# Optimization experiments

Measured on AMD Instinct MI355X. Metric: run time of the kernel, lower is better.

## Reference

```python
import jax, jax.numpy as jnp
import numpy as np

N = 10000        # nodes
E = 160000       # edges (before self-loops)
NFEAT = 256
NHID = 128
H = 4            # heads
NCLASS = 40
NLAYERS = 2
DT = 1.0
ALPHA = 1.0
GAMMA = 1.0
NEG_SLOPE = 0.2  # GATConv leaky_relu slope


def setup_inputs() -> dict:
    key = jax.random.key(0)
    ks = jax.random.split(key, 12)

    def glorot(k, shape):
        fan_in, fan_out = shape[-1], shape[0]
        lim = (6.0 / (fan_in + fan_out)) ** 0.5
        return jax.random.uniform(k, shape, jnp.float32, -lim, lim)

    return {
        "x": jax.random.normal(ks[0], (N, NFEAT), jnp.float32),
        "edge_index": jax.random.randint(ks[1], (2, E), 0, N, jnp.int64),
        "enc_w": glorot(ks[2], (NHID, NFEAT)),
        "enc_b": jnp.zeros((NHID,), jnp.float32),
        "res_w": glorot(ks[3], (H * NHID, NHID)),
        "res_b": jnp.zeros((H * NHID,), jnp.float32),
        "gat_w": glorot(ks[4], (H * NHID, NHID)),
        "att_src": glorot(ks[5], (H, NHID)) * 0.1,
        "att_dst": glorot(ks[6], (H, NHID)) * 0.1,
        "gat_b": jnp.zeros((H * NHID,), jnp.float32),
        "dec_w": glorot(ks[7], (NCLASS, NHID)),
        "dec_b": jnp.zeros((NCLASS,), jnp.float32),
    }


def _gat_conv(x, src, dst, gat_w, att_src, att_dst, gat_b):
    # x: [N, NHID] -> per-head features [N, H, C]
    xh = (x @ gat_w.T).reshape(N, H, NHID)
    a_src = jnp.sum(xh * att_src[None], axis=-1)  # [N, H]
    a_dst = jnp.sum(xh * att_dst[None], axis=-1)  # [N, H]
    e = jax.nn.leaky_relu(a_src[src] + a_dst[dst], NEG_SLOPE)  # [E', H]
    # segment softmax over incoming edges of each destination node
    m = jax.ops.segment_max(e, dst, num_segments=N)            # [N, H]
    e = jnp.exp(e - m[dst])
    s = jax.ops.segment_sum(e, dst, num_segments=N)            # [N, H]
    alpha = e / s[dst]                                          # [E', H]
    msg = xh[src] * alpha[:, :, None]                           # [E', H, C]
    out = jax.ops.segment_sum(msg, dst, num_segments=N)         # [N, H, C]
    return out.reshape(N, H * NHID) + gat_b


def reference(x, edge_index, enc_w, enc_b, res_w, res_b, gat_w,
              att_src, att_dst, gat_b, dec_w, dec_b):
    # add self-loops (GATConv default)
    loop = jnp.arange(N, dtype=edge_index.dtype)
    src = jnp.concatenate([edge_index[0], loop])
    dst = jnp.concatenate([edge_index[1], loop])

    Y = jax.nn.relu(x @ enc_w.T + enc_b)  # [N, NHID]
    X = Y
    for _ in range(NLAYERS):
        conv = _gat_conv(X, src, dst, gat_w, att_src, att_dst, gat_b)  # [N, H*NHID]
        res = X @ res_w.T + res_b                                       # [N, H*NHID]
        # faithful to .view(n_nodes, -1, nheads).mean(-1): [N, NHID, H] -> mean over heads axis
        z = jax.nn.elu(conv + res).reshape(N, NHID, H).mean(axis=-1)    # [N, NHID]
        Y = Y + DT * (z - ALPHA * Y - GAMMA * X)
        X = X + DT * Y
    return X @ dec_w.T + dec_b  # [N, NCLASS]
```

## Files before the change

### kernel.cpp

```cpp
#include <hip/hip_runtime.h>
#include <math.h>

#define NN 10000
#define EE 160000
#define EP 170000
#define NFEAT 256
#define NHID 128
#define NH 4
#define HF 512
#define NCLASS 40

typedef __attribute__((ext_vector_type(8))) short bf8;
typedef __attribute__((ext_vector_type(8))) unsigned short u16x8;
typedef __attribute__((ext_vector_type(4))) float f4;

__device__ __forceinline__ float leaky02(float x) { return x >= 0.0f ? x : 0.2f * x; }

__device__ __forceinline__ unsigned short f2bf(float f) {
    unsigned u = __builtin_bit_cast(unsigned, f);
    unsigned r = (u + 0x7FFF + ((u >> 16) & 1)) >> 16;
    return (unsigned short)r;
}
__device__ __forceinline__ float bf2f(unsigned short h) {
    return __builtin_bit_cast(float, (unsigned)h << 16);
}

__device__ __forceinline__ int swz(int row, int c) {
    return ((((c >> 3) ^ (row & 7)) << 3) | (c & 7));
}

__device__ __forceinline__ void gl_lds16(const unsigned short* g, unsigned short* l)
{
    __builtin_amdgcn_global_load_lds(
        (const __attribute__((address_space(1))) unsigned int*)g,
        (__attribute__((address_space(3))) unsigned int*)l, 16, 0, 0);
}

#define CVT_EL 136192
#define CVT_B  67
#define TOT_B  188

__global__ __launch_bounds__(256)
void fused0_k(const float* __restrict__ gat_w, const float* __restrict__ res_w,
              const float* __restrict__ dec_w,
              const float* __restrict__ res_b, const float* __restrict__ gat_b,
              const int* __restrict__ ei,
              unsigned short* __restrict__ fwhi, unsigned short* __restrict__ dwhi,
              float* __restrict__ biasRG, int* __restrict__ cnt)
{
    int bId = blockIdx.x, t = threadIdx.x;
    if (bId < CVT_B) {
        int iu = bId * 256 + t;
        int i = iu * 8;
        if (i >= CVT_EL) return;
        const float* src; unsigned short* ph; int j;
        if (i < 131072) { j = i;          ph = fwhi;
                          src = (j < 65536) ? (gat_w + j) : (res_w + j - 65536); }
        else            { j = i - 131072; ph = dwhi; src = dec_w + j; }
        int row = j >> 7, c = j & 127;
        float4 v0 = *(const float4*)src, v1 = *(const float4*)(src + 4);
        float vv[8] = {v0.x, v0.y, v0.z, v0.w, v1.x, v1.y, v1.z, v1.w};
        unsigned short hs[8];
#pragma unroll
        for (int k = 0; k < 8; ++k) hs[k] = f2bf(vv[k]);
        *(u16x8*)(ph + row * 128 + swz(row, c)) = *(u16x8*)hs;
    } else if (bId == CVT_B) {
        biasRG[t]       = res_b[t]       + gat_b[t];
        biasRG[t + 256] = res_b[t + 256] + gat_b[t + 256];
    } else {
        for (int e = (bId - CVT_B - 1) * 256 + t; e < EP; e += (TOT_B - CVT_B - 1) * 256) {
            int d = (e < EE) ? ei[EE + e] : (e - EE);
            atomicAdd(&cnt[d], 1);
        }
    }
}

template<int MODE, int KTILES, int MERGE, bool F32>
__global__ __launch_bounds__(256)
void gemm3_k(const void* __restrict__ Ap, const void* __restrict__ Bp,
             const float* __restrict__ bias, float* __restrict__ outF,
             unsigned short* __restrict__ outH, unsigned short* __restrict__ outL,
             float* __restrict__ aS, float* __restrict__ aD,
             const float* __restrict__ attS, const float* __restrict__ attD, int M,
             const int* __restrict__ ei, const int* __restrict__ cnt,
             int* __restrict__ row_ptr, int* __restrict__ cursor, int* __restrict__ csr)
{
    constexpr int K = KTILES * 128;
    __shared__ __align__(16) unsigned short smem[2 * 64 * 128];
    const int tid = threadIdx.x;

    if (MERGE && blockIdx.y == gridDim.y - 1) {
        if (MERGE == 1) {
            if (blockIdx.x != 0) return;
            int* smi = (int*)smem;
            int i0 = tid * 40, i1 = min(i0 + 40, NN);
            int part = 0;
            for (int i = i0; i < i1; ++i) part += cnt[i];
            smi[tid] = part;
            __syncthreads();
            for (int off = 1; off < 256; off <<= 1) {
                int v = (tid >= off) ? smi[tid - off] : 0;
                __syncthreads();
                smi[tid] += v;
                __syncthreads();
            }
            int run = smi[tid] - part;
            for (int i = i0; i < i1; ++i) { row_ptr[i] = run; run += cnt[i]; }
            if (tid == 255) row_ptr[NN] = run;
        } else {
            int stride = gridDim.x * 256;
            for (int e = blockIdx.x * 256 + tid; e < EP; e += stride) {
                int s, d;
                if (e < EE) { s = ei[e]; d = ei[EE + e]; } else { s = e - EE; d = s; }
                int pos = row_ptr[d] + atomicAdd(&cursor[d], 1);
                csr[pos] = s;
            }
        }
        return;
    }

    unsigned short* sA = smem;
    unsigned short* sB = smem + 8192;

    const int lane = tid & 63, wv = tid >> 6;
    const int wr = (wv >> 1) * 32, wc = (wv & 1) * 32;
    const int bm = blockIdx.x * 64, bn = blockIdx.y * 64;
    const int r16 = lane & 15, q4 = lane >> 4;

    f4 acc[2][2];
#pragma unroll
    for (int i = 0; i < 2; ++i)
#pragma unroll
        for (int j = 0; j < 2; ++j) acc[i][j] = (f4){0.f, 0.f, 0.f, 0.f};

    const int ra0 = wr + r16;
    const int rb0 = wc + r16;

    for (int kt = 0; kt < KTILES; ++kt) {
        if (kt) __syncthreads();
        if (!F32) {
            const unsigned short* A = (const unsigned short*)Ap;
            const unsigned short* B = (const unsigned short*)Bp;
#pragma unroll
            for (int j = 0; j < 4; ++j) {
                int i = tid + j * 256;
                int row = i >> 4, u = i & 15;
                int arow = min(bm + row, M - 1);
                size_t ga = (size_t)arow * K + kt * 128 + u * 8;
                size_t gb = (size_t)(bn + row) * K + kt * 128 + u * 8;
                int lb = (wv * 64 + j * 256) * 8;
                gl_lds16(A + ga, sA + lb);
                gl_lds16(B + gb, sB + lb);
            }
        } else {
            const float* A = (const float*)Ap;
            const float* B = (const float*)Bp;
#pragma unroll
            for (int j = 0; j < 4; ++j) {
                int i = tid + j * 256;
                int row = i >> 4, u = i & 15;
                int arow = min(bm + row, M - 1);
                const float* pa = A + (size_t)arow * K + kt * 128 + u * 8;
                const float* pb = B + (size_t)(bn + row) * K + kt * 128 + u * 8;
                float4 a0 = *(const float4*)pa, a1 = *(const float4*)(pa + 4);
                float4 b0 = *(const float4*)pb, b1 = *(const float4*)(pb + 4);
                float av[8] = {a0.x, a0.y, a0.z, a0.w, a1.x, a1.y, a1.z, a1.w};
                float bv[8] = {b0.x, b0.y, b0.z, b0.w, b1.x, b1.y, b1.z, b1.w};
                unsigned short ha[8], hb[8];
#pragma unroll
                for (int k = 0; k < 8; ++k) { ha[k] = f2bf(av[k]); hb[k] = f2bf(bv[k]); }
                int off = row * 128 + ((u ^ (row & 7)) * 8);
                *(u16x8*)(sA + off) = *(u16x8*)ha;
                *(u16x8*)(sB + off) = *(u16x8*)hb;
            }
        }
        __syncthreads();

#pragma unroll
        for (int ks = 0; ks < 4; ++ks) {
            int u = ks * 4 + q4;
            int oa0 = ra0 * 128 + ((u ^ (ra0 & 7)) * 8);
            int ob0 = rb0 * 128 + ((u ^ (rb0 & 7)) * 8);
            int oa1 = oa0 + 16 * 128;
            int ob1 = ob0 + 16 * 128;
            bf8 A0 = *(const bf8*)(sA + oa0);
            bf8 A1 = *(const bf8*)(sA + oa1);
            bf8 B0 = *(const bf8*)(sB + ob0);
            bf8 B1 = *(const bf8*)(sB + ob1);

            acc[0][0] = __builtin_amdgcn_mfma_f32_16x16x32_bf16(A0, B0, acc[0][0], 0, 0, 0);
            acc[0][1] = __builtin_amdgcn_mfma_f32_16x16x32_bf16(A0, B1, acc[0][1], 0, 0, 0);
            acc[1][0] = __builtin_amdgcn_mfma_f32_16x16x32_bf16(A1, B0, acc[1][0], 0, 0, 0);
            acc[1][1] = __builtin_amdgcn_mfma_f32_16x16x32_bf16(A1, B1, acc[1][1], 0, 0, 0);
        }
    }

    const int rbase = q4 * 4;

    if (MODE == 0) {
#pragma unroll
        for (int i = 0; i < 2; ++i)
#pragma unroll
            for (int j = 0; j < 2; ++j)
#pragma unroll
                for (int r = 0; r < 4; ++r) {
                    int row = bm + wr + i * 16 + rbase + r;
                    int col = bn + wc + j * 16 + r16;
                    if (row >= M || col >= NCLASS) continue;
                    outF[(size_t)row * NCLASS + col] = acc[i][j][r] + bias[col];
                }
        return;
    }

    __syncthreads();
    float* sC = (float*)smem;
#pragma unroll
    for (int i = 0; i < 2; ++i)
#pragma unroll
        for (int j = 0; j < 2; ++j)
#pragma unroll
            for (int r = 0; r < 4; ++r)
                sC[(wr + i * 16 + rbase + r) * 65 + (wc + j * 16 + r16)] = acc[i][j][r];
    __syncthreads();

    int row = tid >> 2, seg = tid & 3, c0 = seg * 16;
    int grow = bm + row;
    if (grow < M) {
        float v[16];
#pragma unroll
        for (int k = 0; k < 16; ++k) v[k] = sC[row * 65 + c0 + k];

        if (MODE == 1) {
            unsigned short hs[16];
#pragma unroll
            for (int k = 0; k < 16; ++k)
                hs[k] = f2bf(fmaxf(v[k] + bias[bn + c0 + k], 0.0f));
#pragma unroll
            for (int uu = 0; uu < 2; ++uu) {
                int ug = (bn + c0) / 8 + uu;
                int pu = ug ^ (grow & 7);
                *(u16x8*)(outH + (size_t)grow * 128 + pu * 8) = *(u16x8*)(hs + uu * 8);
            }
        } else {
            if (bn < 512) {
                unsigned short hs[16];
#pragma unroll
                for (int k = 0; k < 16; ++k) hs[k] = f2bf(v[k]);
                *(u16x8*)(outH + (size_t)grow * 512 + bn + c0)     = *(u16x8*)hs;
                *(u16x8*)(outH + (size_t)grow * 512 + bn + c0 + 8) = *(u16x8*)(hs + 8);
                float ps = 0.0f, pd = 0.0f;
#pragma unroll
                for (int k = 0; k < 16; ++k) {
                    ps = fmaf(v[k], attS[bn + c0 + k], ps);
                    pd = fmaf(v[k], attD[bn + c0 + k], pd);
                }
                ps += __shfl_xor(ps, 1); ps += __shfl_xor(ps, 2);
                pd += __shfl_xor(pd, 1); pd += __shfl_xor(pd, 2);
                if (seg == 0) {
                    int h = bn >> 7;
                    atomicAdd(&aS[grow * 4 + h], ps);
                    atomicAdd(&aD[grow * 4 + h], pd);
                }
            } else {
                unsigned short hs[16];
#pragma unroll
                for (int k = 0; k < 16; ++k) hs[k] = f2bf(v[k] + bias[bn - 512 + c0 + k]);
                *(u16x8*)(outL + (size_t)grow * 512 + (bn - 512) + c0)     = *(u16x8*)hs;
                *(u16x8*)(outL + (size_t)grow * 512 + (bn - 512) + c0 + 8) = *(u16x8*)(hs + 8);
            }
        }
    }
}

__global__ __launch_bounds__(256)
void agg_k(const int* __restrict__ row_ptr, const int* __restrict__ csr,
           const float* __restrict__ a_src, const float* __restrict__ a_dst,
           const unsigned short* __restrict__ xh_b, const unsigned short* __restrict__ resb,
           unsigned short* __restrict__ Xhi)
{
    int bx = blockIdx.x;
    int h  = bx / 2500;
    int ng = bx - h * 2500;
    int wv = threadIdx.x >> 6, lane = threadIdx.x & 63;
    int d = ng * 4 + wv;
    int beg = row_ptr[d], end = row_ptr[d + 1];
    int eg = lane >> 4, c16 = lane & 15;
    int cb = h * 128 + c16 * 8;
    float ad = a_dst[d * 4 + h];
    u16x8 rv = *(const u16x8*)(resb + (size_t)d * HF + cb);

    float acc[8];
#pragma unroll
    for (int k = 0; k < 8; ++k) acc[k] = 0.0f;
    float ssum = 0.0f;

    int e = beg;
    for (; e + 16 <= end; e += 16) {
        int sv[4]; float w[4]; u16x8 v[4];
#pragma unroll
        for (int q = 0; q < 4; ++q) sv[q] = csr[e + q * 4 + eg];
#pragma unroll
        for (int q = 0; q < 4; ++q) v[q] = *(const u16x8*)(xh_b + (size_t)sv[q] * HF + cb);
#pragma unroll
        for (int q = 0; q < 4; ++q) {
            w[q] = __expf(leaky02(a_src[sv[q] * 4 + h] + ad));
            ssum += w[q];
        }
#pragma unroll
        for (int q = 0; q < 4; ++q)
#pragma unroll
            for (int k = 0; k < 8; ++k) acc[k] = fmaf(w[q], bf2f(v[q][k]), acc[k]);
    }
    for (; e + 4 <= end; e += 4) {
        int s = csr[e + eg];
        u16x8 v = *(const u16x8*)(xh_b + (size_t)s * HF + cb);
        float w = __expf(leaky02(a_src[s * 4 + h] + ad));
        ssum += w;
#pragma unroll
        for (int k = 0; k < 8; ++k) acc[k] = fmaf(w, bf2f(v[k]), acc[k]);
    }
    if (e + eg < end) {
        int s = csr[e + eg];
        u16x8 v = *(const u16x8*)(xh_b + (size_t)s * HF + cb);
        float w = __expf(leaky02(a_src[s * 4 + h] + ad));
        ssum += w;
#pragma unroll
        for (int k = 0; k < 8; ++k) acc[k] = fmaf(w, bf2f(v[k]), acc[k]);
    }

#pragma unroll
    for (int off = 16; off <= 32; off <<= 1) {
        ssum += __shfl_xor(ssum, off);
#pragma unroll
        for (int k = 0; k < 8; ++k) acc[k] += __shfl_xor(acc[k], off);
    }

    float inv = 1.0f / ssum;
    float uv[8];
#pragma unroll
    for (int k = 0; k < 8; ++k) {
        float v = fmaf(acc[k], inv, bf2f(rv[k]));
        uv[k] = (v > 0.0f) ? v : expm1f(v);
    }
    float z0 = (uv[0] + uv[1] + uv[2] + uv[3]) * 0.25f;
    float z1 = (uv[4] + uv[5] + uv[6] + uv[7]) * 0.25f;
    if (eg == 0) {
        int col = h * 32 + c16 * 2;
        unsigned short h0b = f2bf(z0), h1b = f2bf(z1);
        size_t idx = (size_t)d * NHID + swz(d, col);
        *(unsigned*)(Xhi + idx) = ((unsigned)h1b << 16) | h0b;
    }
}

extern "C" void kernel_launch(void* const* d_in, const int* in_sizes, int n_in,
                              void* d_out, int out_size, void* d_ws, size_t ws_size,
                              hipStream_t stream)
{
    const float* x       = (const float*)d_in[0];
    const int*   ei      = (const int*)d_in[1];
    const float* enc_w   = (const float*)d_in[2];
    const float* enc_b   = (const float*)d_in[3];
    const float* res_w   = (const float*)d_in[4];
    const float* res_b   = (const float*)d_in[5];
    const float* gat_w   = (const float*)d_in[6];
    const float* att_src = (const float*)d_in[7];
    const float* att_dst = (const float*)d_in[8];
    const float* gat_b   = (const float*)d_in[9];
    const float* dec_w   = (const float*)d_in[10];
    const float* dec_b   = (const float*)d_in[11];
    float* out = (float*)d_out;

    char* p = (char*)d_ws;
    auto alloc = [&](size_t bytes) -> void* {
        void* r = (void*)p;
        p += (bytes + 255) & ~(size_t)255;
        return r;
    };
    float* biasRG = (float*)alloc(512 * 4);
    unsigned short* xh_b = (unsigned short*)alloc(5120000 * 2);
    unsigned short* resb = (unsigned short*)alloc(5120000 * 2);
    unsigned short* Xhi  = (unsigned short*)alloc(1280000 * 2);
    unsigned short* fwhi = (unsigned short*)alloc(1024 * 128 * 2);
    int* row_ptr = (int*)alloc(10004 * 4);
    int* csr     = (int*)alloc(170000 * 4);
    char* zbase = p;
    unsigned short* dwhi = (unsigned short*)alloc(8192 * 2);
    int* cnt    = (int*)alloc(10000 * 4);
    int* cursor = (int*)alloc(10000 * 4);
    float* aS1  = (float*)alloc(40000 * 4);
    float* aD1  = (float*)alloc(40000 * 4);
    float* aS2  = (float*)alloc(40000 * 4);
    float* aD2  = (float*)alloc(40000 * 4);
    size_t zbytes = (size_t)(p - zbase);

    hipMemsetAsync(zbase, 0, zbytes, stream);

    fused0_k<<<TOT_B, 256, 0, stream>>>(
        gat_w, res_w, dec_w, res_b, gat_b, ei, fwhi, dwhi, biasRG, cnt);

    gemm3_k<1, 2, 1, true><<<dim3(157, 3), 256, 0, stream>>>(
        x, enc_w, enc_b, nullptr, Xhi, nullptr, nullptr, nullptr, nullptr, nullptr, NN,
        nullptr, cnt, row_ptr, nullptr, nullptr);

    gemm3_k<2, 1, 2, false><<<dim3(157, 17), 256, 0, stream>>>(
        Xhi, fwhi, biasRG, nullptr, xh_b, resb, aS1, aD1, att_src, att_dst, NN,
        ei, nullptr, row_ptr, cursor, csr);
    agg_k<<<10000, 256, 0, stream>>>(row_ptr, csr, aS1, aD1, xh_b, resb, Xhi);

    gemm3_k<2, 1, 0, false><<<dim3(157, 16), 256, 0, stream>>>(
        Xhi, fwhi, biasRG, nullptr, xh_b, resb, aS2, aD2, att_src, att_dst, NN,
        nullptr, nullptr, nullptr, nullptr, nullptr);
    agg_k<<<10000, 256, 0, stream>>>(row_ptr, csr, aS2, aD2, xh_b, resb, Xhi);

    gemm3_k<0, 1, 0, false><<<dim3(157, 1), 256, 0, stream>>>(
        Xhi, dwhi, dec_b, out, nullptr, nullptr, nullptr, nullptr, nullptr, nullptr, NN,
        nullptr, nullptr, nullptr, nullptr, nullptr);
}
```

Measured before the change: 206.5 us.

## Drop memset launch, widen GEMM N-tile to 128, write attention logits directly

Removes the hipMemsetAsync by zeroing the degree counters inside fused0_k, using 8 blocks that each own a 1250-node range. Every one of these blocks scans all edges but only counts destinations in its own range. The decoder weight padding is also zeroed in fused0_k. The GEMM gains a BN template parameter, and the hidden GEMMs use 128-wide N tiles, so each block covers a full head. That lets the attention logits be stored with plain writes instead of atomics, halves the number of column blocks, and increases A-tile reuse. The CSR cursor is now initialised during the prefix scan, so the scatter step no longer adds row_ptr. The aS/aD buffers are shared between the two layers. The trade-off is more redundant edge reads for counting and a larger LDS and register footprint per GEMM block.

```diff
diff --git a/kernel.cpp b/kernel.cpp
--- a/kernel.cpp
+++ b/kernel.cpp
@@ -38,7 +38,7 @@
 
 #define CVT_EL 136192
 #define CVT_B  67
-#define TOT_B  188
+#define TOT_B  76
 
 __global__ __launch_bounds__(256)
 void fused0_k(const float* __restrict__ gat_w, const float* __restrict__ res_w,
@@ -67,15 +67,22 @@
     } else if (bId == CVT_B) {
         biasRG[t]       = res_b[t]       + gat_b[t];
         biasRG[t + 256] = res_b[t + 256] + gat_b[t + 256];
+        u16x8 z = {0, 0, 0, 0, 0, 0, 0, 0};
+        for (int i = t; i < 384; i += 256)
+            *(u16x8*)(dwhi + 40 * 128 + i * 8) = z;
     } else {
-        for (int e = (bId - CVT_B - 1) * 256 + t; e < EP; e += (TOT_B - CVT_B - 1) * 256) {
+        int b = bId - CVT_B - 1;
+        int lo = b * 1250;
+        for (int i = t; i < 1250; i += 256) cnt[lo + i] = 0;
+        __syncthreads();
+        for (int e = t; e < EP; e += 256) {
             int d = (e < EE) ? ei[EE + e] : (e - EE);
-            atomicAdd(&cnt[d], 1);
-        }
-    }
-}
-
-template<int MODE, int KTILES, int MERGE, bool F32>
+            if ((unsigned)(d - lo) < 1250u) atomicAdd(&cnt[d], 1);
+        }
+    }
+}
+
+template<int MODE, int KTILES, int MERGE, bool F32, int BN>
 __global__ __launch_bounds__(256)
 void gemm3_k(const void* __restrict__ Ap, const void* __restrict__ Bp,
              const float* __restrict__ bias, float* __restrict__ outF,
@@ -85,8 +92,12 @@
              const int* __restrict__ ei, const int* __restrict__ cnt,
              int* __restrict__ row_ptr, int* __restrict__ cursor, int* __restrict__ csr)
 {
-    constexpr int K = KTILES * 128;
-    __shared__ __align__(16) unsigned short smem[2 * 64 * 128];
+    constexpr int K  = KTILES * 128;
+    constexpr int JT = BN / 32;
+    constexpr int TU = 1024 + BN * 16;
+    constexpr int CW = BN / 4;
+    constexpr int BNP = BN + 4;
+    __shared__ __align__(16) unsigned short smem[8192 + BN * 128];
     const int tid = threadIdx.x;
 
     if (MERGE && blockIdx.y == gridDim.y - 1) {
@@ -105,14 +116,16 @@
                 __syncthreads();
             }
             int run = smi[tid] - part;
-            for (int i = i0; i < i1; ++i) { row_ptr[i] = run; run += cnt[i]; }
+            for (int i = i0; i < i1; ++i) {
+                row_ptr[i] = run; cursor[i] = run; run += cnt[i];
+            }
             if (tid == 255) row_ptr[NN] = run;
         } else {
             int stride = gridDim.x * 256;
             for (int e = blockIdx.x * 256 + tid; e < EP; e += stride) {
                 int s, d;
                 if (e < EE) { s = ei[e]; d = ei[EE + e]; } else { s = e - EE; d = s; }
-                int pos = row_ptr[d] + atomicAdd(&cursor[d], 1);
+                int pos = atomicAdd(&cursor[d], 1);
                 csr[pos] = s;
             }
         }
@@ -123,15 +136,15 @@
     unsigned short* sB = smem + 8192;
 
     const int lane = tid & 63, wv = tid >> 6;
-    const int wr = (wv >> 1) * 32, wc = (wv & 1) * 32;
-    const int bm = blockIdx.x * 64, bn = blockIdx.y * 64;
+    const int wr = (wv >> 1) * 32, wc = (wv & 1) * (BN / 2);
+    const int bm = blockIdx.x * 64, bn = blockIdx.y * BN;
     const int r16 = lane & 15, q4 = lane >> 4;
 
-    f4 acc[2][2];
+    f4 acc[2][JT];
 #pragma unroll
     for (int i = 0; i < 2; ++i)
 #pragma unroll
-        for (int j = 0; j < 2; ++j) acc[i][j] = (f4){0.f, 0.f, 0.f, 0.f};
+        for (int j = 0; j < JT; ++j) acc[i][j] = (f4){0.f, 0.f, 0.f, 0.f};
 
     const int ra0 = wr + r16;
     const int rb0 = wc + r16;
@@ -142,36 +155,39 @@
             const unsigned short* A = (const unsigned short*)Ap;
             const unsigned short* B = (const unsigned short*)Bp;
 #pragma unroll
-            for (int j = 0; j < 4; ++j) {
+            for (int j = 0; j < TU / 256; ++j) {
                 int i = tid + j * 256;
-                int row = i >> 4, u = i & 15;
-                int arow = min(bm + row, M - 1);
-                size_t ga = (size_t)arow * K + kt * 128 + u * 8;
-                size_t gb = (size_t)(bn + row) * K + kt * 128 + u * 8;
-                int lb = (wv * 64 + j * 256) * 8;
-                gl_lds16(A + ga, sA + lb);
-                gl_lds16(B + gb, sB + lb);
+                if (j < 4) {
+                    int row = i >> 4, u = i & 15;
+                    size_t ga = (size_t)min(bm + row, M - 1) * K + kt * 128 + u * 8;
+                    int lb = (wv * 64 + j * 256) * 8;
+                    gl_lds16(A + ga, sA + lb);
+                } else {
+                    int ib = i - 1024;
+                    int row = ib >> 4, u = ib & 15;
+                    size_t gb = (size_t)(bn + row) * K + kt * 128 + u * 8;
+                    int lb = (wv * 64 + (j - 4) * 256) * 8;
+                    gl_lds16(B + gb, sB + lb);
+                }
             }
         } else {
             const float* A = (const float*)Ap;
             const float* B = (const float*)Bp;
 #pragma unroll
-            for (int j = 0; j < 4; ++j) {
+            for (int j = 0; j < TU / 256; ++j) {
                 int i = tid + j * 256;
-                int row = i >> 4, u = i & 15;
-                int arow = min(bm + row, M - 1);
-                const float* pa = A + (size_t)arow * K + kt * 128 + u * 8;
-                const float* pb = B + (size_t)(bn + row) * K + kt * 128 + u * 8;
-                float4 a0 = *(const float4*)pa, a1 = *(const float4*)(pa + 4);
-                float4 b0 = *(const float4*)pb, b1 = *(const float4*)(pb + 4);
-                float av[8] = {a0.x, a0.y, a0.z, a0.w, a1.x, a1.y, a1.z, a1.w};
-                float bv[8] = {b0.x, b0.y, b0.z, b0.w, b1.x, b1.y, b1.z, b1.w};
-                unsigned short ha[8], hb[8];
-#pragma unroll
-                for (int k = 0; k < 8; ++k) { ha[k] = f2bf(av[k]); hb[k] = f2bf(bv[k]); }
+                const float* src; unsigned short* dst; int row, u;
+                if (j < 4) { row = i >> 4; u = i & 15; dst = sA;
+                             src = A + (size_t)min(bm + row, M - 1) * K + kt * 128 + u * 8; }
+                else       { int ib = i - 1024; row = ib >> 4; u = ib & 15; dst = sB;
+                             src = B + (size_t)(bn + row) * K + kt * 128 + u * 8; }
+                float4 v0 = *(const float4*)src, v1 = *(const float4*)(src + 4);
+                float vv[8] = {v0.x, v0.y, v0.z, v0.w, v1.x, v1.y, v1.z, v1.w};
+                unsigned short hs[8];
+#pragma unroll
+                for (int k = 0; k < 8; ++k) hs[k] = f2bf(vv[k]);
                 int off = row * 128 + ((u ^ (row & 7)) * 8);
-                *(u16x8*)(sA + off) = *(u16x8*)ha;
-                *(u16x8*)(sB + off) = *(u16x8*)hb;
+                *(u16x8*)(dst + off) = *(u16x8*)hs;
             }
         }
         __syncthreads();
@@ -179,19 +195,19 @@
 #pragma unroll
         for (int ks = 0; ks < 4; ++ks) {
             int u = ks * 4 + q4;
-            int oa0 = ra0 * 128 + ((u ^ (ra0 & 7)) * 8);
-            int ob0 = rb0 * 128 + ((u ^ (rb0 & 7)) * 8);
-            int oa1 = oa0 + 16 * 128;
-            int ob1 = ob0 + 16 * 128;
-            bf8 A0 = *(const bf8*)(sA + oa0);
-            bf8 A1 = *(const bf8*)(sA + oa1);
-            bf8 B0 = *(const bf8*)(sB + ob0);
-            bf8 B1 = *(const bf8*)(sB + ob1);
-
-            acc[0][0] = __builtin_amdgcn_mfma_f32_16x16x32_bf16(A0, B0, acc[0][0], 0, 0, 0);
-            acc[0][1] = __builtin_amdgcn_mfma_f32_16x16x32_bf16(A0, B1, acc[0][1], 0, 0, 0);
-            acc[1][0] = __builtin_amdgcn_mfma_f32_16x16x32_bf16(A1, B0, acc[1][0], 0, 0, 0);
-            acc[1][1] = __builtin_amdgcn_mfma_f32_16x16x32_bf16(A1, B1, acc[1][1], 0, 0, 0);
+            bf8 Af[2], Bf[JT];
+#pragma unroll
+            for (int i = 0; i < 2; ++i)
+                Af[i] = *(const bf8*)(sA + (ra0 + 16 * i) * 128 + ((u ^ (ra0 & 7)) * 8));
+#pragma unroll
+            for (int j = 0; j < JT; ++j)
+                Bf[j] = *(const bf8*)(sB + (rb0 + 16 * j) * 128 + ((u ^ (rb0 & 7)) * 8));
+#pragma unroll
+            for (int i = 0; i < 2; ++i)
+#pragma unroll
+                for (int j = 0; j < JT; ++j)
+                    acc[i][j] = __builtin_amdgcn_mfma_f32_16x16x32_bf16(
+                        Af[i], Bf[j], acc[i][j], 0, 0, 0);
         }
     }
 
@@ -201,7 +217,7 @@
 #pragma unroll
         for (int i = 0; i < 2; ++i)
 #pragma unroll
-            for (int j = 0; j < 2; ++j)
+            for (int j = 0; j < JT; ++j)
 #pragma unroll
                 for (int r = 0; r < 4; ++r) {
                     int row = bm + wr + i * 16 + rbase + r;
@@ -217,40 +233,42 @@
 #pragma unroll
     for (int i = 0; i < 2; ++i)
 #pragma unroll
-        for (int j = 0; j < 2; ++j)
+        for (int j = 0; j < JT; ++j)
 #pragma unroll
             for (int r = 0; r < 4; ++r)
-                sC[(wr + i * 16 + rbase + r) * 65 + (wc + j * 16 + r16)] = acc[i][j][r];
+                sC[(wr + i * 16 + rbase + r) * BNP + (wc + j * 16 + r16)] = acc[i][j][r];
     __syncthreads();
 
-    int row = tid >> 2, seg = tid & 3, c0 = seg * 16;
+    int row = tid >> 2, seg = tid & 3, c0 = seg * CW;
     int grow = bm + row;
     if (grow < M) {
-        float v[16];
-#pragma unroll
-        for (int k = 0; k < 16; ++k) v[k] = sC[row * 65 + c0 + k];
+        float v[CW];
+#pragma unroll
+        for (int k = 0; k < CW; ++k) v[k] = sC[row * BNP + c0 + k];
 
         if (MODE == 1) {
-            unsigned short hs[16];
-#pragma unroll
-            for (int k = 0; k < 16; ++k)
+            unsigned short hs[CW];
+#pragma unroll
+            for (int k = 0; k < CW; ++k)
                 hs[k] = f2bf(fmaxf(v[k] + bias[bn + c0 + k], 0.0f));
 #pragma unroll
-            for (int uu = 0; uu < 2; ++uu) {
+            for (int uu = 0; uu < CW / 8; ++uu) {
                 int ug = (bn + c0) / 8 + uu;
                 int pu = ug ^ (grow & 7);
                 *(u16x8*)(outH + (size_t)grow * 128 + pu * 8) = *(u16x8*)(hs + uu * 8);
             }
         } else {
             if (bn < 512) {
-                unsigned short hs[16];
-#pragma unroll
-                for (int k = 0; k < 16; ++k) hs[k] = f2bf(v[k]);
-                *(u16x8*)(outH + (size_t)grow * 512 + bn + c0)     = *(u16x8*)hs;
-                *(u16x8*)(outH + (size_t)grow * 512 + bn + c0 + 8) = *(u16x8*)(hs + 8);
+                unsigned short hs[CW];
+#pragma unroll
+                for (int k = 0; k < CW; ++k) hs[k] = f2bf(v[k]);
+#pragma unroll
+                for (int uu = 0; uu < CW / 8; ++uu)
+                    *(u16x8*)(outH + (size_t)grow * 512 + bn + c0 + uu * 8)
+                        = *(u16x8*)(hs + uu * 8);
                 float ps = 0.0f, pd = 0.0f;
 #pragma unroll
-                for (int k = 0; k < 16; ++k) {
+                for (int k = 0; k < CW; ++k) {
                     ps = fmaf(v[k], attS[bn + c0 + k], ps);
                     pd = fmaf(v[k], attD[bn + c0 + k], pd);
                 }
@@ -258,15 +276,18 @@
                 pd += __shfl_xor(pd, 1); pd += __shfl_xor(pd, 2);
                 if (seg == 0) {
                     int h = bn >> 7;
-                    atomicAdd(&aS[grow * 4 + h], ps);
-                    atomicAdd(&aD[grow * 4 + h], pd);
+                    aS[grow * 4 + h] = ps;
+                    aD[grow * 4 + h] = pd;
                 }
             } else {
-                unsigned short hs[16];
-#pragma unroll
-                for (int k = 0; k < 16; ++k) hs[k] = f2bf(v[k] + bias[bn - 512 + c0 + k]);
-                *(u16x8*)(outL + (size_t)grow * 512 + (bn - 512) + c0)     = *(u16x8*)hs;
-                *(u16x8*)(outL + (size_t)grow * 512 + (bn - 512) + c0 + 8) = *(u16x8*)(hs + 8);
+                unsigned short hs[CW];
+#pragma unroll
+                for (int k = 0; k < CW; ++k)
+                    hs[k] = f2bf(v[k] + bias[bn - 512 + c0 + k]);
+#pragma unroll
+                for (int uu = 0; uu < CW / 8; ++uu)
+                    *(u16x8*)(outL + (size_t)grow * 512 + (bn - 512) + c0 + uu * 8)
+                        = *(u16x8*)(hs + uu * 8);
             }
         }
     }
@@ -381,38 +402,32 @@
     unsigned short* resb = (unsigned short*)alloc(5120000 * 2);
     unsigned short* Xhi  = (unsigned short*)alloc(1280000 * 2);
     unsigned short* fwhi = (unsigned short*)alloc(1024 * 128 * 2);
+    unsigned short* dwhi = (unsigned short*)alloc(8192 * 2);
     int* row_ptr = (int*)alloc(10004 * 4);
     int* csr     = (int*)alloc(170000 * 4);
-    char* zbase = p;
-    unsigned short* dwhi = (unsigned short*)alloc(8192 * 2);
-    int* cnt    = (int*)alloc(10000 * 4);
-    int* cursor = (int*)alloc(10000 * 4);
-    float* aS1  = (float*)alloc(40000 * 4);
-    float* aD1  = (float*)alloc(40000 * 4);
-    float* aS2  = (float*)alloc(40000 * 4);
-    float* aD2  = (float*)alloc(40000 * 4);
-    size_t zbytes = (size_t)(p - zbase);
-
-    hipMemsetAsync(zbase, 0, zbytes, stream);
+    int* cnt     = (int*)alloc(10000 * 4);
+    int* cursor  = (int*)alloc(10000 * 4);
+    float* aS    = (float*)alloc(40000 * 4);
+    float* aD    = (float*)alloc(40000 * 4);
 
     fused0_k<<<TOT_B, 256, 0, stream>>>(
         gat_w, res_w, dec_w, res_b, gat_b, ei, fwhi, dwhi, biasRG, cnt);
 
-    gemm3_k<1, 2, 1, true><<<dim3(157, 3), 256, 0, stream>>>(
+    gemm3_k<1, 2, 1, true, 128><<<dim3(157, 2), 256, 0, stream>>>(
         x, enc_w, enc_b, nullptr, Xhi, nullptr, nullptr, nullptr, nullptr, nullptr, NN,
-        nullptr, cnt, row_ptr, nullptr, nullptr);
-
-    gemm3_k<2, 1, 2, false><<<dim3(157, 17), 256, 0, stream>>>(
-        Xhi, fwhi, biasRG, nullptr, xh_b, resb, aS1, aD1, att_src, att_dst, NN,
-        ei, nullptr, row_ptr, cursor, csr);
-    agg_k<<<10000, 256, 0, stream>>>(row_ptr, csr, aS1, aD1, xh_b, resb, Xhi);
-
-    gemm3_k<2, 1, 0, false><<<dim3(157, 16), 256, 0, stream>>>(
-        Xhi, fwhi, biasRG, nullptr, xh_b, resb, aS2, aD2, att_src, att_dst, NN,
+        nullptr, cnt, row_ptr, cursor, nullptr);
+
+    gemm3_k<2, 1, 2, false, 128><<<dim3(157, 9), 256, 0, stream>>>(
+        Xhi, fwhi, biasRG, nullptr, xh_b, resb, aS, aD, att_src, att_dst, NN,
+        ei, nullptr, nullptr, cursor, csr);
+    agg_k<<<10000, 256, 0, stream>>>(row_ptr, csr, aS, aD, xh_b, resb, Xhi);
+
+    gemm3_k<2, 1, 0, false, 128><<<dim3(157, 8), 256, 0, stream>>>(
+        Xhi, fwhi, biasRG, nullptr, xh_b, resb, aS, aD, att_src, att_dst, NN,
         nullptr, nullptr, nullptr, nullptr, nullptr);
-    agg_k<<<10000, 256, 0, stream>>>(row_ptr, csr, aS2, aD2, xh_b, resb, Xhi);
-
-    gemm3_k<0, 1, 0, false><<<dim3(157, 1), 256, 0, stream>>>(
+    agg_k<<<10000, 256, 0, stream>>>(row_ptr, csr, aS, aD, xh_b, resb, Xhi);
+
+    gemm3_k<0, 1, 0, false, 64><<<dim3(157, 1), 256, 0, stream>>>(
         Xhi, dwhi, dec_b, out, nullptr, nullptr, nullptr, nullptr, nullptr, nullptr, NN,
         nullptr, nullptr, nullptr, nullptr, nullptr);
 }
```

Result: slower. 455.2 us (+120.4%).
